# Optimization experiments

Measured on AMD Instinct MI355X. Metric: run time of the kernel, lower is better.

The kernel has to match this reference:

```python
import jax, jax.numpy as jnp
import numpy as np

B, L, D_MODEL = 2, 1024, 1024
D_STATE, D_CONV, EXPAND, HEADDIM = 64, 4, 2, 64
D_INNER = EXPAND * D_MODEL              # 2048
NHEADS = D_INNER // HEADDIM             # 32
NGROUPS = 1
CONV_DIM = D_INNER + 2 * NGROUPS * D_STATE            # 2176
D_IN_PROJ = 2 * D_INNER + 2 * NGROUPS * D_STATE + NHEADS  # 4256
RMS_EPS = 1e-6      # block nn.RMSNorm eps
GATED_EPS = 1e-5    # Mamba2 RMSNormGated eps

def _rmsnorm(x, w, eps):
    return x * jax.lax.rsqrt(jnp.mean(x * x, axis=-1, keepdims=True) + eps) * w

def _silu(x):
    return x * jax.nn.sigmoid(x)

def _mamba2(x, W_in, conv_w, conv_b, dt_bias, A_log, D_param, ssm_norm_w, W_out):
    b, l, _ = x.shape
    zxbcdt = x @ W_in.T                                   # (b,l,D_IN_PROJ)
    z = zxbcdt[..., :D_INNER]
    xBC = zxbcdt[..., D_INNER:D_INNER + CONV_DIM]
    dt = zxbcdt[..., D_INNER + CONV_DIM:]                 # (b,l,H)
    # depthwise causal conv1d (kernel D_CONV) + silu
    pad = jnp.pad(xBC, ((0, 0), (D_CONV - 1, 0), (0, 0)))
    conv = conv_b + sum(pad[:, i:i + l, :] * conv_w[:, i] for i in range(D_CONV))
    xBC = _silu(conv)
    xs = xBC[..., :D_INNER].reshape(b, l, NHEADS, HEADDIM)
    Bm = xBC[..., D_INNER:D_INNER + D_STATE]              # (b,l,N), ngroups=1
    Cm = xBC[..., D_INNER + D_STATE:]                     # (b,l,N)
    dt = jax.nn.softplus(dt + dt_bias)                    # (b,l,H)
    dA = jnp.exp(dt * (-jnp.exp(A_log)))                  # (b,l,H)
    dtx = dt[..., None] * xs                              # (b,l,H,P)

    def step(h, inp):
        dA_t, dtx_t, B_t, C_t = inp
        h = h * dA_t[:, :, None, None] + dtx_t[..., None] * B_t[:, None, None, :]
        y_t = jnp.einsum('bhpn,bn->bhp', h, C_t)
        return h, y_t

    h0 = jnp.zeros((b, NHEADS, HEADDIM, D_STATE), x.dtype)
    _, ys = jax.lax.scan(step, h0, (dA.transpose(1, 0, 2), dtx.transpose(1, 0, 2, 3),
                                    Bm.transpose(1, 0, 2), Cm.transpose(1, 0, 2)))
    y = ys.transpose(1, 0, 2, 3) + xs * D_param[None, None, :, None]
    y = y.reshape(b, l, D_INNER)
    y = _rmsnorm(y * _silu(z), ssm_norm_w, GATED_EPS)     # RMSNormGated, norm_before_gate=False
    return y @ W_out.T

def _block(x, x_d, norm_w, W_in, conv_w, conv_b, dt_bias, A_log, D_param, ssm_norm_w, W_out, w1, w2):
    # dual_residual=True, residual_scale=1.0, dropout is identity (eval)
    x_ln = _rmsnorm(x, norm_w, RMS_EPS)
    x_f = _mamba2(x_ln, W_in, conv_w, conv_b, dt_bias, A_log, D_param, ssm_norm_w, W_out)
    x_a = x + x_f
    x_f_scaled = x_f
    x_ln = _rmsnorm(x_a, norm_w, RMS_EPS)
    g = x_ln @ w1.T
    x_f = (g * jax.nn.sigmoid(g)) * (x_ln @ w2.T)         # SwiGLU
    x_a = x_a + x_f
    x_f_scaled = x_f_scaled + x_f
    return x_a, x_d + x_f_scaled

def setup_inputs() -> dict:
    key = jax.random.key(0)
    ks = jax.random.split(key, 12)
    dt = jax.random.uniform(ks[6], (NHEADS,), minval=1e-3, maxval=0.1)
    return {
        'x': jax.random.normal(ks[0], (B, L, D_MODEL), jnp.float32),
        'x_d': jax.random.normal(ks[1], (B, L, D_MODEL), jnp.float32),
        'norm_w': jnp.ones((D_MODEL,), jnp.float32),
        'W_in': jax.random.normal(ks[2], (D_IN_PROJ, D_MODEL), jnp.float32) * (D_MODEL ** -0.5),
        'conv_w': jax.random.normal(ks[3], (CONV_DIM, D_CONV), jnp.float32) * 0.2,
        'conv_b': jnp.zeros((CONV_DIM,), jnp.float32),
        'dt_bias': dt + jnp.log(-jnp.expm1(-dt)),   # inverse softplus of dt
        'A_log': jnp.log(jax.random.uniform(ks[7], (NHEADS,), minval=1.0, maxval=16.0)),
        'D_param': jnp.ones((NHEADS,), jnp.float32),
        'ssm_norm_w': jnp.ones((D_INNER,), jnp.float32),
        'W_out': jax.random.normal(ks[4], (D_MODEL, D_INNER), jnp.float32) * (D_INNER ** -0.5),
        'w1': jax.random.normal(ks[8], (D_MODEL, D_MODEL), jnp.float32) * (D_MODEL ** -0.5),
        'w2': jax.random.normal(ks[9], (D_MODEL, D_MODEL), jnp.float32) * (D_MODEL ** -0.5),
    }

def reference(x, x_d, norm_w, W_in, conv_w, conv_b, dt_bias, A_log, D_param, ssm_norm_w, W_out, w1, w2):
    return _block(x, x_d, norm_w, W_in, conv_w, conv_b, dt_bias, A_log, D_param, ssm_norm_w, W_out, w1, w2)
```

## Files before the change

kernel.cpp:

```cpp
#include <hip/hip_runtime.h>

typedef unsigned short u16;
typedef __attribute__((ext_vector_type(8))) short bf16x8;
typedef __attribute__((ext_vector_type(4))) float f32x4;

#define B_      2
#define L_      1024
#define DM      1024
#define DI      2048
#define NH      32
#define HD      64
#define DSTATE  64
#define CONVD   2176
#define DPROJ   4256
#define ZXS     4352

__device__ __forceinline__ u16 f2bf(float f) {
  union { float f; unsigned u; } v; v.f = f;
  unsigned r = v.u + 0x7fffu + ((v.u >> 16) & 1u);
  return (u16)(r >> 16);
}
__device__ __forceinline__ float bf2f(u16 b) {
  union { unsigned u; float f; } v; v.u = ((unsigned)b) << 16;
  return v.f;
}

__device__ __forceinline__ void load_lds16(const void* g, void* l) {
  __builtin_amdgcn_global_load_lds(
      (const __attribute__((address_space(1))) void*)g,
      (__attribute__((address_space(3))) void*)l, 16, 0, 0);
}

template<int P> __device__ __forceinline__ void wait_prefetch() {
  if constexpr (P == 4)      asm volatile("s_waitcnt vmcnt(4)\n\ts_barrier" ::: "memory");
  else if constexpr (P == 6) asm volatile("s_waitcnt vmcnt(6)\n\ts_barrier" ::: "memory");
  else if constexpr (P == 8) asm volatile("s_waitcnt vmcnt(8)\n\ts_barrier" ::: "memory");
}

__device__ __forceinline__ float block_reduce_sum256(float v) {
  #pragma unroll
  for (int off = 32; off > 0; off >>= 1) v += __shfl_down(v, off, 64);
  __shared__ float red[4];
  int lane = threadIdx.x & 63, w = threadIdx.x >> 6;
  if (lane == 0) red[w] = v;
  __syncthreads();
  return red[0] + red[1] + red[2] + red[3];
}

__global__ __launch_bounds__(256) void rms_and_convert(
    const float* __restrict__ x, const float* __restrict__ norm_w, u16* __restrict__ xlnb,
    const float* __restrict__ W_in, const float* __restrict__ W_out,
    const float* __restrict__ w1, const float* __restrict__ w2,
    u16* __restrict__ Winb, u16* __restrict__ Woutb, u16* __restrict__ w12b) {
  if (blockIdx.x < 2048) {
    const int row = blockIdx.x;
    const int c = threadIdx.x << 2;
    float4 v = *(const float4*)(x + (long)row * DM + c);
    float ss = v.x * v.x + v.y * v.y + v.z * v.z + v.w * v.w;
    float tot = block_reduce_sum256(ss);
    float sc = rsqrtf(tot * (1.0f / DM) + 1e-6f);
    float4 wv = *(const float4*)(norm_w + c);
    *(ushort4*)(xlnb + (long)row * DM + c) =
        make_ushort4(f2bf(v.x * sc * wv.x), f2bf(v.y * sc * wv.y),
                     f2bf(v.z * sc * wv.z), f2bf(v.w * sc * wv.w));
    return;
  }
  const long R0 = 4256L * 1024 / 4;
  const long R1 = R0 + 2048L * 1024 / 4;
  long i = (long)(blockIdx.x - 2048) * 256 + threadIdx.x;
  float4 v;
  ushort4* dst;
  if (i < R0) {
    v = ((const float4*)W_in)[i];
    dst = ((ushort4*)Winb) + i;
  } else if (i < R1) {
    long j = i - R0;
    v = ((const float4*)W_out)[j];
    dst = ((ushort4*)Woutb) + j;
  } else {
    long j = i - R1;
    long row = j >> 8;
    const float* s = (row < 1024) ? (w1 + row * 1024) : (w2 + (row - 1024) * 1024);
    v = ((const float4*)s)[j & 255];
    dst = ((ushort4*)w12b) + j;
  }
  *dst = make_ushort4(f2bf(v.x), f2bf(v.y), f2bf(v.z), f2bf(v.w));
}

__global__ __launch_bounds__(256) void add_rms_kernel(
    const float* __restrict__ in1, const float* __restrict__ in2,
    float* __restrict__ sum_out, const float* __restrict__ wt,
    u16* __restrict__ out, float eps) {
  const int row = blockIdx.x;
  const int c = threadIdx.x << 2;
  float4 v = *(const float4*)(in1 + (long)row * DM + c);
  float4 u = *(const float4*)(in2 + (long)row * DM + c);
  v.x += u.x; v.y += u.y; v.z += u.z; v.w += u.w;
  *(float4*)(sum_out + (long)row * DM + c) = v;
  float ss = v.x * v.x + v.y * v.y + v.z * v.z + v.w * v.w;
  float tot = block_reduce_sum256(ss);
  float sc = rsqrtf(tot * (1.0f / DM) + eps);
  float4 wv = *(const float4*)(wt + c);
  *(ushort4*)(out + (long)row * DM + c) =
      make_ushort4(f2bf(v.x * sc * wv.x), f2bf(v.y * sc * wv.y),
                   f2bf(v.z * sc * wv.z), f2bf(v.w * sc * wv.w));
}

template<int NI, int NJ, int OUT>
__global__ __launch_bounds__(256) void gemm_lds(
    const u16* __restrict__ A, const u16* __restrict__ Bw,
    void* __restrict__ Cv, int N, int Nw, int Ksub, int Kstride) {
  constexpr int BM = NI * 32;
  constexpr int BN = NJ * 32;
  __shared__ u16 As[2][BM][64];
  __shared__ u16 Bs[2][BN][64];
  const int tid = threadIdx.x;
  const int lane = tid & 63;
  const int wave = tid >> 6;
  const int ml = lane & 15;
  const int quad = lane >> 4;
  const int wm = (wave & 1) * (NI * 16);
  const int wn = (wave >> 1) * (NJ * 16);
  const long bm = (long)blockIdx.y * BM;
  const long bn = (long)blockIdx.x * BN;
  const long koff = (long)blockIdx.z * Ksub;

  const int lr = lane >> 3;
  const int lc = (lane & 7) ^ lr;

  f32x4 acc[NI][NJ];
  #pragma unroll
  for (int i = 0; i < NI; ++i)
    #pragma unroll
    for (int j = 0; j < NJ; ++j)
      acc[i][j] = (f32x4){0.f, 0.f, 0.f, 0.f};

  auto stage = [&](int kk, int buf) {
    #pragma unroll
    for (int t = 0; t < BM / 32; ++t) {
      const int u = wave * (BM / 32) + t;
      load_lds16(A + (bm + u * 8 + lr) * Kstride + koff + kk + lc * 8, &As[buf][u * 8][0]);
    }
    #pragma unroll
    for (int t = 0; t < BN / 32; ++t) {
      const int u = wave * (BN / 32) + t;
      long brow = bn + u * 8 + lr;
      if (brow >= Nw) brow = Nw - 1;
      load_lds16(Bw + brow * Kstride + koff + kk + lc * 8, &Bs[buf][u * 8][0]);
    }
  };

  stage(0, 0);
  int buf = 0;
  for (int kt = 0; kt < Ksub; kt += 64) {
    if (kt + 64 < Ksub) {
      stage(kt + 64, buf ^ 1);
      wait_prefetch<NI + NJ>();
    } else {
      asm volatile("s_waitcnt vmcnt(0)\n\ts_barrier" ::: "memory");
    }
    #pragma unroll
    for (int ks = 0; ks < 2; ++ks) {
      const int c = ks * 4 + quad;
      const int pc = (c ^ (ml & 7)) << 3;
      bf16x8 af[NI], bfr[NJ];
      #pragma unroll
      for (int i = 0; i < NI; ++i)
        af[i] = *(const bf16x8*)&As[buf][wm + (i << 4) + ml][pc];
      #pragma unroll
      for (int j = 0; j < NJ; ++j)
        bfr[j] = *(const bf16x8*)&Bs[buf][wn + (j << 4) + ml][pc];
      #pragma unroll
      for (int i = 0; i < NI; ++i)
        #pragma unroll
        for (int j = 0; j < NJ; ++j)
          acc[i][j] = __builtin_amdgcn_mfma_f32_16x16x32_bf16(af[i], bfr[j], acc[i][j], 0, 0, 0);
    }
    asm volatile("s_barrier" ::: "memory");
    buf ^= 1;
  }

  const int rquad = quad << 2;
  #pragma unroll
  for (int i = 0; i < NI; ++i) {
    const long gm = bm + wm + (i << 4) + rquad;
    #pragma unroll
    for (int j = 0; j < NJ; ++j) {
      const long gn = bn + wn + (j << 4) + ml;
      #pragma unroll
      for (int r = 0; r < 4; ++r) {
        if constexpr (OUT == 0)
          ((float*)Cv)[(gm + r) * N + gn] = acc[i][j][r];
        else if constexpr (OUT == 1)
          ((u16*)Cv)[(gm + r) * N + gn] = f2bf(acc[i][j][r]);
        else
          atomicAdd(&((float*)Cv)[(gm + r) * N + gn], acc[i][j][r]);
      }
    }
  }
}

__global__ __launch_bounds__(256) void gemm_mlp_final(
    const u16* __restrict__ A, const u16* __restrict__ Bw,
    const float* __restrict__ xa, const float* __restrict__ xd,
    const float* __restrict__ xf, float* __restrict__ out, int K) {
  __shared__ u16 As[2][64][64];
  __shared__ u16 Bs[2][128][64];
  const int tid = threadIdx.x;
  const int lane = tid & 63;
  const int wave = tid >> 6;
  const int ml = lane & 15;
  const int quad = lane >> 4;
  const int wm = (wave & 1) * 32;
  const int wn = (wave >> 1) * 32;
  const long bm = (long)blockIdx.y * 64;
  const long c0 = (long)blockIdx.x * 64;

  const int lr = lane >> 3;
  const int lc = (lane & 7) ^ lr;

  f32x4 acc[2][4];
  #pragma unroll
  for (int i = 0; i < 2; ++i)
    #pragma unroll
    for (int j = 0; j < 4; ++j)
      acc[i][j] = (f32x4){0.f, 0.f, 0.f, 0.f};

  auto stage = [&](int kk, int buf) {
    #pragma unroll
    for (int t = 0; t < 2; ++t) {
      const int u = wave * 2 + t;
      load_lds16(A + (bm + u * 8 + lr) * K + kk + lc * 8, &As[buf][u * 8][0]);
    }
    #pragma unroll
    for (int t = 0; t < 4; ++t) {
      const int u = wave * 4 + t;
      const int r = u * 8 + lr;
      const long grow = (r < 64) ? (c0 + r) : (1024 + c0 + (r - 64));
      load_lds16(Bw + grow * K + kk + lc * 8, &Bs[buf][u * 8][0]);
    }
  };

  stage(0, 0);
  int buf = 0;
  for (int kt = 0; kt < K; kt += 64) {
    if (kt + 64 < K) {
      stage(kt + 64, buf ^ 1);
      wait_prefetch<6>();
    } else {
      asm volatile("s_waitcnt vmcnt(0)\n\ts_barrier" ::: "memory");
    }
    #pragma unroll
    for (int ks = 0; ks < 2; ++ks) {
      const int c = ks * 4 + quad;
      const int pc = (c ^ (ml & 7)) << 3;
      bf16x8 af[2], bfr[4];
      #pragma unroll
      for (int i = 0; i < 2; ++i)
        af[i] = *(const bf16x8*)&As[buf][wm + (i << 4) + ml][pc];
      #pragma unroll
      for (int j = 0; j < 2; ++j) {
        bfr[j]     = *(const bf16x8*)&Bs[buf][wn + (j << 4) + ml][pc];
        bfr[j + 2] = *(const bf16x8*)&Bs[buf][64 + wn + (j << 4) + ml][pc];
      }
      #pragma unroll
      for (int i = 0; i < 2; ++i)
        #pragma unroll
        for (int j = 0; j < 4; ++j)
          acc[i][j] = __builtin_amdgcn_mfma_f32_16x16x32_bf16(af[i], bfr[j], acc[i][j], 0, 0, 0);
    }
    asm volatile("s_barrier" ::: "memory");
    buf ^= 1;
  }

  float* out1 = out + (long)B_ * L_ * DM;
  const int rquad = quad << 2;
  #pragma unroll
  for (int i = 0; i < 2; ++i) {
    const long gm = bm + wm + (i << 4) + rquad;
    #pragma unroll
    for (int jj = 0; jj < 2; ++jj) {
      const long col = c0 + wn + (jj << 4) + ml;
      #pragma unroll
      for (int r = 0; r < 4; ++r) {
        float g = acc[i][jj][r];
        float h = acc[i][jj + 2][r];
        float e = (g / (1.f + expf(-g))) * h;
        long o = (gm + r) * DM + col;
        out[o]  = xa[o] + e;
        out1[o] = xd[o] + xf[o] + e;
      }
    }
  }
}

__global__ __launch_bounds__(256) void conv_silu_kernel(
    const u16* __restrict__ zx, const float* __restrict__ cw,
    const float* __restrict__ cb, u16* __restrict__ xc) {
  int idx = blockIdx.x * 256 + threadIdx.x;
  if (idx >= 2048 * 544) return;
  const int c4 = (idx % 544) << 2;
  const int row = idx / 544;
  const int t = row & (L_ - 1);
  float4 acc = *(const float4*)(cb + c4);
  float4 w0 = *(const float4*)(cw + (c4 + 0) * 4);
  float4 w1v = *(const float4*)(cw + (c4 + 1) * 4);
  float4 w2v = *(const float4*)(cw + (c4 + 2) * 4);
  float4 w3v = *(const float4*)(cw + (c4 + 3) * 4);
  const float wts[4][4] = {{w0.x, w0.y, w0.z, w0.w},
                           {w1v.x, w1v.y, w1v.z, w1v.w},
                           {w2v.x, w2v.y, w2v.z, w2v.w},
                           {w3v.x, w3v.y, w3v.z, w3v.w}};
  #pragma unroll
  for (int i = 0; i < 4; ++i) {
    int tau = t - 3 + i;
    if (tau >= 0) {
      ushort4 xb = *(const ushort4*)(zx + (long)(row - t + tau) * ZXS + DI + c4);
      acc.x = fmaf(bf2f(xb.x), wts[0][i], acc.x);
      acc.y = fmaf(bf2f(xb.y), wts[1][i], acc.y);
      acc.z = fmaf(bf2f(xb.z), wts[2][i], acc.z);
      acc.w = fmaf(bf2f(xb.w), wts[3][i], acc.w);
    }
  }
  acc.x = acc.x / (1.f + expf(-acc.x));
  acc.y = acc.y / (1.f + expf(-acc.y));
  acc.z = acc.z / (1.f + expf(-acc.z));
  acc.w = acc.w / (1.f + expf(-acc.w));
  *(ushort4*)(xc + (long)row * CONVD + c4) =
      make_ushort4(f2bf(acc.x), f2bf(acc.y), f2bf(acc.z), f2bf(acc.w));
}

__global__ __launch_bounds__(256) void ssd_chunk_kernel(
    const u16* __restrict__ xc, const u16* __restrict__ zx,
    const float* __restrict__ dt_bias, const float* __restrict__ A_log,
    u16* __restrict__ yss, float* __restrict__ Sbuf,
    float* __restrict__ EGbuf, float* __restrict__ Lam) {
  const int c = blockIdx.x & 15;
  const int h = (blockIdx.x >> 4) & 31;
  const int b = blockIdx.x >> 9;
  const int bh = b * NH + h;
  const long crow = (long)b * L_ + c * 64;
  const int tid = threadIdx.x, lane = tid & 63, wave = tid >> 6;

  __shared__ u16 Cs[64][72], Bs[64][72], Xt[64][72], Btw[64][72], Ms[64][72];
  __shared__ float Gs[64], wjL[64], dtL[64];

  if (wave == 0) {
    float draw = bf2f(zx[(crow + lane) * ZXS + (DI + CONVD) + h]) + dt_bias[h];
    float dt = (draw > 20.f) ? draw : log1pf(expf(draw));
    float g = -expf(A_log[h]) * dt;
    float G = g;
    #pragma unroll
    for (int off = 1; off < 64; off <<= 1) {
      float t = __shfl_up(G, off, 64);
      if (lane >= off) G += t;
    }
    float G63 = __shfl(G, 63, 64);
    Gs[lane] = G;
    wjL[lane] = expf(G63 - G) * dt;
    dtL[lane] = dt;
    EGbuf[(bh * 16 + c) * 64 + lane] = expf(G);
    if (lane == 63) Lam[bh * 16 + c] = expf(G63);
  }
  __syncthreads();
  for (int idx = tid; idx < 1024; idx += 256) {
    int r = idx >> 4, c4 = (idx & 15) << 2;
    const u16* row = xc + (crow + r) * CONVD;
    ushort4 xv = *(const ushort4*)(row + h * HD + c4);
    Xt[c4 + 0][r] = xv.x; Xt[c4 + 1][r] = xv.y;
    Xt[c4 + 2][r] = xv.z; Xt[c4 + 3][r] = xv.w;
    ushort4 bv = *(const ushort4*)(row + DI + c4);
    *(ushort4*)&Bs[r][c4] = bv;
    float w = wjL[r];
    Btw[c4 + 0][r] = f2bf(bf2f(bv.x) * w); Btw[c4 + 1][r] = f2bf(bf2f(bv.y) * w);
    Btw[c4 + 2][r] = f2bf(bf2f(bv.z) * w); Btw[c4 + 3][r] = f2bf(bf2f(bv.w) * w);
    *(ushort4*)&Cs[r][c4] = *(const ushort4*)(row + DI + DSTATE + c4);
  }
  __syncthreads();

  const int mrow = wave * 16 + (lane & 15);
  const int quad = lane >> 4;
  f32x4 accE[4];
  #pragma unroll
  for (int j = 0; j < 4; ++j) accE[j] = (f32x4){0.f, 0.f, 0.f, 0.f};
  #pragma unroll
  for (int ks = 0; ks < 2; ++ks) {
    int k0 = ks * 32 + quad * 8;
    bf16x8 a = *(const bf16x8*)&Cs[mrow][k0];
    #pragma unroll
    for (int j = 0; j < 4; ++j) {
      bf16x8 bfr = *(const bf16x8*)&Bs[j * 16 + (lane & 15)][k0];
      accE[j] = __builtin_amdgcn_mfma_f32_16x16x32_bf16(a, bfr, accE[j], 0, 0, 0);
    }
  }
  #pragma unroll
  for (int j = 0; j < 4; ++j) {
    int jc = j * 16 + (lane & 15);
    float Gj = Gs[jc], dtj = dtL[jc];
    #pragma unroll
    for (int r = 0; r < 4; ++r) {
      int ir = wave * 16 + quad * 4 + r;
      float v = (ir >= jc) ? accE[j][r] * expf(Gs[ir] - Gj) * dtj : 0.f;
      Ms[ir][jc] = f2bf(v);
    }
  }
  __syncthreads();
  f32x4 accY[4], accS[4];
  #pragma unroll
  for (int j = 0; j < 4; ++j) { accY[j] = (f32x4){0.f,0.f,0.f,0.f}; accS[j] = (f32x4){0.f,0.f,0.f,0.f}; }
  #pragma unroll
  for (int ks = 0; ks < 2; ++ks) {
    int k0 = ks * 32 + quad * 8;
    bf16x8 aM = *(const bf16x8*)&Ms[mrow][k0];
    bf16x8 aX = *(const bf16x8*)&Xt[mrow][k0];
    #pragma unroll
    for (int j = 0; j < 4; ++j) {
      bf16x8 bX = *(const bf16x8*)&Xt[j * 16 + (lane & 15)][k0];
      bf16x8 bB = *(const bf16x8*)&Btw[j * 16 + (lane & 15)][k0];
      accY[j] = __builtin_amdgcn_mfma_f32_16x16x32_bf16(aM, bX, accY[j], 0, 0, 0);
      accS[j] = __builtin_amdgcn_mfma_f32_16x16x32_bf16(aX, bB, accS[j], 0, 0, 0);
    }
  }
  float* Sc = Sbuf + (long)(bh * 16 + c) * 4096;
  #pragma unroll
  for (int j = 0; j < 4; ++j) {
    int col = j * 16 + (lane & 15);
    #pragma unroll
    for (int r = 0; r < 4; ++r) {
      int mr = wave * 16 + quad * 4 + r;
      yss[(crow + mr) * DI + h * HD + col] = f2bf(accY[j][r]);
      Sc[mr * 64 + col] = accS[j][r];
    }
  }
}

__global__ __launch_bounds__(256) void ssd_combine_kernel(
    float* __restrict__ Sbuf, const float* __restrict__ Lam) {
  const int bh = blockIdx.x >> 4;
  const int e = (blockIdx.x & 15) * 256 + threadIdx.x;
  float* base = Sbuf + (long)bh * 16 * 4096 + e;
  const float* lamp = Lam + bh * 16;
  float H = 0.f;
  for (int cc = 0; cc < 16; ++cc) {
    float lam = lamp[cc];
    float v = base[cc * 4096];
    base[cc * 4096] = H;
    H = fmaf(lam, H, v);
  }
}

__global__ __launch_bounds__(256) void ssd_final_kernel(
    const u16* __restrict__ xc, const float* __restrict__ Sbuf,
    const float* __restrict__ EGbuf, const float* __restrict__ Dp,
    u16* __restrict__ yss) {
  const int c = blockIdx.x & 15;
  const int h = (blockIdx.x >> 4) & 31;
  const int b = blockIdx.x >> 9;
  const int bh = b * NH + h;
  const long crow = (long)b * L_ + c * 64;
  const int tid = threadIdx.x, lane = tid & 63, wave = tid >> 6;
  __shared__ u16 Csc[64][72], Hs[64][72];
  __shared__ float egL[64];
  if (tid < 64) egL[tid] = EGbuf[(bh * 16 + c) * 64 + tid];
  __syncthreads();
  const float* Sc = Sbuf + (long)(bh * 16 + c) * 4096;
  for (int idx = tid; idx < 1024; idx += 256) {
    int r = idx >> 4, c4 = (idx & 15) << 2;
    float4 hv = *(const float4*)(Sc + r * 64 + c4);
    *(ushort4*)&Hs[r][c4] = make_ushort4(f2bf(hv.x), f2bf(hv.y), f2bf(hv.z), f2bf(hv.w));
    float eg = egL[r];
    ushort4 cv = *(const ushort4*)(xc + (crow + r) * CONVD + DI + DSTATE + c4);
    *(ushort4*)&Csc[r][c4] = make_ushort4(f2bf(bf2f(cv.x) * eg), f2bf(bf2f(cv.y) * eg),
                                          f2bf(bf2f(cv.z) * eg), f2bf(bf2f(cv.w) * eg));
  }
  __syncthreads();
  const int mrow = wave * 16 + (lane & 15);
  const int quad = lane >> 4;
  f32x4 acc[4];
  #pragma unroll
  for (int j = 0; j < 4; ++j) acc[j] = (f32x4){0.f, 0.f, 0.f, 0.f};
  #pragma unroll
  for (int ks = 0; ks < 2; ++ks) {
    int k0 = ks * 32 + quad * 8;
    bf16x8 a = *(const bf16x8*)&Csc[mrow][k0];
    #pragma unroll
    for (int j = 0; j < 4; ++j) {
      bf16x8 bfr = *(const bf16x8*)&Hs[j * 16 + (lane & 15)][k0];
      acc[j] = __builtin_amdgcn_mfma_f32_16x16x32_bf16(a, bfr, acc[j], 0, 0, 0);
    }
  }
  const float Dh = Dp[h];
  #pragma unroll
  for (int j = 0; j < 4; ++j) {
    int p = j * 16 + (lane & 15);
    #pragma unroll
    for (int r = 0; r < 4; ++r) {
      int ir = wave * 16 + quad * 4 + r;
      long o = (crow + ir) * DI + h * HD + p;
      float xval = bf2f(xc[(crow + ir) * CONVD + h * HD + p]);
      yss[o] = f2bf(bf2f(yss[o]) + acc[j][r] + Dh * xval);
    }
  }
}

__global__ __launch_bounds__(256) void gated_rms_kernel(
    const u16* __restrict__ y, const u16* __restrict__ zx,
    const float* __restrict__ wt, u16* __restrict__ out,
    float* __restrict__ xf_zero) {
  const int row = blockIdx.x;
  const int c = threadIdx.x << 3;
  const u16* yr = y + (long)row * DI + c;
  const u16* zr = zx + (long)row * ZXS + c;
  *(float4*)(xf_zero + (long)row * DM + (threadIdx.x << 2)) = make_float4(0.f, 0.f, 0.f, 0.f);
  float v[8];
  float ss = 0.f;
  #pragma unroll
  for (int i = 0; i < 8; i += 4) {
    ushort4 y4 = *(const ushort4*)(yr + i);
    ushort4 z4 = *(const ushort4*)(zr + i);
    const float zz[4] = {bf2f(z4.x), bf2f(z4.y), bf2f(z4.z), bf2f(z4.w)};
    const float yy[4] = {bf2f(y4.x), bf2f(y4.y), bf2f(y4.z), bf2f(y4.w)};
    #pragma unroll
    for (int j = 0; j < 4; ++j) {
      float sg = zz[j] / (1.f + expf(-zz[j]));
      float val = yy[j] * sg;
      v[i + j] = val;
      ss += val * val;
    }
  }
  float tot = block_reduce_sum256(ss);
  float sc = rsqrtf(tot * (1.0f / DI) + 1e-5f);
  const float* wr = wt + c;
  *(ushort4*)(out + (long)row * DI + c) =
      make_ushort4(f2bf(v[0] * sc * wr[0]), f2bf(v[1] * sc * wr[1]),
                   f2bf(v[2] * sc * wr[2]), f2bf(v[3] * sc * wr[3]));
  *(ushort4*)(out + (long)row * DI + c + 4) =
      make_ushort4(f2bf(v[4] * sc * wr[4]), f2bf(v[5] * sc * wr[5]),
                   f2bf(v[6] * sc * wr[6]), f2bf(v[7] * sc * wr[7]));
}

extern "C" void kernel_launch(void* const* d_in, const int* in_sizes, int n_in,
                              void* d_out, int out_size, void* d_ws, size_t ws_size,
                              hipStream_t stream) {
  const float* x        = (const float*)d_in[0];
  const float* x_d      = (const float*)d_in[1];
  const float* norm_w   = (const float*)d_in[2];
  const float* W_in     = (const float*)d_in[3];
  const float* conv_w   = (const float*)d_in[4];
  const float* conv_b   = (const float*)d_in[5];
  const float* dt_bias  = (const float*)d_in[6];
  const float* A_log    = (const float*)d_in[7];
  const float* D_param  = (const float*)d_in[8];
  const float* ssm_w    = (const float*)d_in[9];
  const float* W_out    = (const float*)d_in[10];
  const float* w1       = (const float*)d_in[11];
  const float* w2       = (const float*)d_in[12];
  float* out = (float*)d_out;

  char* wsc = (char*)d_ws;
  size_t off = 0;
  auto alloc = [&](size_t n) { char* p = wsc + off; off += (n + 255) & ~(size_t)255; return p; };
  u16*   zx   = (u16*)alloc((size_t)2048 * ZXS * 2);
  u16*   xc   = (u16*)alloc((size_t)2048 * 2176 * 2);
  u16*   yss  = (u16*)alloc((size_t)2048 * 2048 * 2);
  float* xf   = (float*)alloc((size_t)2048 * 1024 * 4);
  float* xa   = (float*)alloc((size_t)2048 * 1024 * 4);
  float* Sbuf = (float*)alloc((size_t)64 * 16 * 4096 * 4);
  float* EGbuf= (float*)alloc((size_t)65536 * 4);
  float* Lam  = (float*)alloc((size_t)1024 * 4);
  u16* xlnb   = (u16*)alloc((size_t)2048 * 1024 * 2);
  u16* ygnb   = (u16*)alloc((size_t)2048 * 2048 * 2);
  u16* xln2b  = (u16*)alloc((size_t)2048 * 1024 * 2);
  u16* Winb   = (u16*)alloc((size_t)4256 * 1024 * 2);
  u16* Woutb  = (u16*)alloc((size_t)1024 * 2048 * 2);
  u16* w12b   = (u16*)alloc((size_t)2048 * 1024 * 2);

  rms_and_convert<<<2048 + 8352, 256, 0, stream>>>(x, norm_w, xlnb,
      W_in, W_out, w1, w2, Winb, Woutb, w12b);
  gemm_lds<4, 2, 1><<<dim3(68, 16), 256, 0, stream>>>(xlnb, Winb, zx, ZXS, 4256, 1024, 1024);
  conv_silu_kernel<<<(2048 * 544 + 255) / 256, 256, 0, stream>>>(zx, conv_w, conv_b, xc);
  ssd_chunk_kernel<<<1024, 256, 0, stream>>>(xc, zx, dt_bias, A_log, yss, Sbuf, EGbuf, Lam);
  ssd_combine_kernel<<<1024, 256, 0, stream>>>(Sbuf, Lam);
  ssd_final_kernel<<<1024, 256, 0, stream>>>(xc, Sbuf, EGbuf, D_param, yss);
  gated_rms_kernel<<<2048, 256, 0, stream>>>(yss, zx, ssm_w, ygnb, xf);
  gemm_lds<2, 2, 2><<<dim3(16, 32, 2), 256, 0, stream>>>(ygnb, Woutb, xf, 1024, 1024, 1024, 2048);
  add_rms_kernel<<<2048, 256, 0, stream>>>(x, xf, xa, norm_w, xln2b, 1e-6f);
  gemm_mlp_final<<<dim3(16, 32), 256, 0, stream>>>(xln2b, w12b, xa, x_d, xf, out, 1024);
}
```

Measured before the change: 255.0 us.

## Fuse conv, chunked SSD, state carry and output into one decoupled-lookback kernel

Replaces the separate conv+silu, chunk, combine and final SSD kernels with a single kernel. It computes the causal conv inline into shared memory, takes chunk order from an atomic ticket, and passes inter-chunk states through a global carry buffer guarded by acquire/release flags. It also drops the xa residual buffer by recomputing x + xf in the final MLP epilogue. This removes several launches and the round trips through xc, Sbuf and EGbuf, at the cost of a serial chain of flag waits across the 16 chunks per head and redundant conv halo loads.

```diff
diff --git a/kernel.cpp b/kernel.cpp
--- a/kernel.cpp
+++ b/kernel.cpp
@@ -89,14 +89,12 @@
 
 __global__ __launch_bounds__(256) void add_rms_kernel(
     const float* __restrict__ in1, const float* __restrict__ in2,
-    float* __restrict__ sum_out, const float* __restrict__ wt,
-    u16* __restrict__ out, float eps) {
+    const float* __restrict__ wt, u16* __restrict__ out, float eps) {
   const int row = blockIdx.x;
   const int c = threadIdx.x << 2;
   float4 v = *(const float4*)(in1 + (long)row * DM + c);
   float4 u = *(const float4*)(in2 + (long)row * DM + c);
   v.x += u.x; v.y += u.y; v.z += u.z; v.w += u.w;
-  *(float4*)(sum_out + (long)row * DM + c) = v;
   float ss = v.x * v.x + v.y * v.y + v.z * v.z + v.w * v.w;
   float tot = block_reduce_sum256(ss);
   float sc = rsqrtf(tot * (1.0f / DM) + eps);
@@ -202,7 +200,7 @@
 
 __global__ __launch_bounds__(256) void gemm_mlp_final(
     const u16* __restrict__ A, const u16* __restrict__ Bw,
-    const float* __restrict__ xa, const float* __restrict__ xd,
+    const float* __restrict__ x0, const float* __restrict__ xd,
     const float* __restrict__ xf, float* __restrict__ out, int K) {
   __shared__ u16 As[2][64][64];
   __shared__ u16 Bs[2][128][64];
@@ -287,63 +285,34 @@
         float h = acc[i][jj + 2][r];
         float e = (g / (1.f + expf(-g))) * h;
         long o = (gm + r) * DM + col;
-        out[o]  = xa[o] + e;
-        out1[o] = xd[o] + xf[o] + e;
-      }
-    }
-  }
-}
-
-__global__ __launch_bounds__(256) void conv_silu_kernel(
-    const u16* __restrict__ zx, const float* __restrict__ cw,
-    const float* __restrict__ cb, u16* __restrict__ xc) {
-  int idx = blockIdx.x * 256 + threadIdx.x;
-  if (idx >= 2048 * 544) return;
-  const int c4 = (idx % 544) << 2;
-  const int row = idx / 544;
-  const int t = row & (L_ - 1);
-  float4 acc = *(const float4*)(cb + c4);
-  float4 w0 = *(const float4*)(cw + (c4 + 0) * 4);
-  float4 w1v = *(const float4*)(cw + (c4 + 1) * 4);
-  float4 w2v = *(const float4*)(cw + (c4 + 2) * 4);
-  float4 w3v = *(const float4*)(cw + (c4 + 3) * 4);
-  const float wts[4][4] = {{w0.x, w0.y, w0.z, w0.w},
-                           {w1v.x, w1v.y, w1v.z, w1v.w},
-                           {w2v.x, w2v.y, w2v.z, w2v.w},
-                           {w3v.x, w3v.y, w3v.z, w3v.w}};
-  #pragma unroll
-  for (int i = 0; i < 4; ++i) {
-    int tau = t - 3 + i;
-    if (tau >= 0) {
-      ushort4 xb = *(const ushort4*)(zx + (long)(row - t + tau) * ZXS + DI + c4);
-      acc.x = fmaf(bf2f(xb.x), wts[0][i], acc.x);
-      acc.y = fmaf(bf2f(xb.y), wts[1][i], acc.y);
-      acc.z = fmaf(bf2f(xb.z), wts[2][i], acc.z);
-      acc.w = fmaf(bf2f(xb.w), wts[3][i], acc.w);
-    }
-  }
-  acc.x = acc.x / (1.f + expf(-acc.x));
-  acc.y = acc.y / (1.f + expf(-acc.y));
-  acc.z = acc.z / (1.f + expf(-acc.z));
-  acc.w = acc.w / (1.f + expf(-acc.w));
-  *(ushort4*)(xc + (long)row * CONVD + c4) =
-      make_ushort4(f2bf(acc.x), f2bf(acc.y), f2bf(acc.z), f2bf(acc.w));
-}
-
-__global__ __launch_bounds__(256) void ssd_chunk_kernel(
-    const u16* __restrict__ xc, const u16* __restrict__ zx,
-    const float* __restrict__ dt_bias, const float* __restrict__ A_log,
-    u16* __restrict__ yss, float* __restrict__ Sbuf,
-    float* __restrict__ EGbuf, float* __restrict__ Lam) {
-  const int c = blockIdx.x & 15;
-  const int h = (blockIdx.x >> 4) & 31;
-  const int b = blockIdx.x >> 9;
+        float f = xf[o];
+        out[o]  = x0[o] + f + e;
+        out1[o] = xd[o] + f + e;
+      }
+    }
+  }
+}
+
+__global__ __launch_bounds__(256) void ssd_fused_kernel(
+    const u16* __restrict__ zx, const float* __restrict__ dt_bias,
+    const float* __restrict__ A_log, const float* __restrict__ cw,
+    const float* __restrict__ cb, const float* __restrict__ Dp,
+    u16* __restrict__ yss, float* __restrict__ carry,
+    int* __restrict__ flags, int* __restrict__ ticket) {
+  __shared__ u16 Cs[64][72], Bs[64][72], Xt[64][72], Btw[64][72], Ms[64][72];
+  __shared__ float Gs[64], wjL[64], dtL[64], egL[64];
+  __shared__ int tickL;
+  const int tid = threadIdx.x, lane = tid & 63, wave = tid >> 6;
+
+  if (tid == 0) tickL = atomicAdd(ticket, 1);
+  __syncthreads();
+  const int tick = tickL;
+  const int c = tick & 15;
+  const int h = (tick >> 4) & 31;
+  const int b = tick >> 9;
   const int bh = b * NH + h;
-  const long crow = (long)b * L_ + c * 64;
-  const int tid = threadIdx.x, lane = tid & 63, wave = tid >> 6;
-
-  __shared__ u16 Cs[64][72], Bs[64][72], Xt[64][72], Btw[64][72], Ms[64][72];
-  __shared__ float Gs[64], wjL[64], dtL[64];
+  const long zrow0 = (long)b * L_;
+  const long crow = zrow0 + c * 64;
 
   if (wave == 0) {
     float draw = bf2f(zx[(crow + lane) * ZXS + (DI + CONVD) + h]) + dt_bias[h];
@@ -357,28 +326,64 @@
     }
     float G63 = __shfl(G, 63, 64);
     Gs[lane] = G;
+    egL[lane] = expf(G);
     wjL[lane] = expf(G63 - G) * dt;
     dtL[lane] = dt;
-    EGbuf[(bh * 16 + c) * 64 + lane] = expf(G);
-    if (lane == 63) Lam[bh * 16 + c] = expf(G63);
   }
   __syncthreads();
-  for (int idx = tid; idx < 1024; idx += 256) {
-    int r = idx >> 4, c4 = (idx & 15) << 2;
-    const u16* row = xc + (crow + r) * CONVD;
-    ushort4 xv = *(const ushort4*)(row + h * HD + c4);
-    Xt[c4 + 0][r] = xv.x; Xt[c4 + 1][r] = xv.y;
-    Xt[c4 + 2][r] = xv.z; Xt[c4 + 3][r] = xv.w;
-    ushort4 bv = *(const ushort4*)(row + DI + c4);
-    *(ushort4*)&Bs[r][c4] = bv;
-    float w = wjL[r];
-    Btw[c4 + 0][r] = f2bf(bf2f(bv.x) * w); Btw[c4 + 1][r] = f2bf(bf2f(bv.y) * w);
-    Btw[c4 + 2][r] = f2bf(bf2f(bv.z) * w); Btw[c4 + 3][r] = f2bf(bf2f(bv.w) * w);
-    *(ushort4*)&Cs[r][c4] = *(const ushort4*)(row + DI + DSTATE + c4);
+
+  for (int idx = tid; idx < 3072; idx += 256) {
+    int r = idx / 48;
+    int g = idx % 48;
+    int t = c * 64 + r;
+    long zcol;
+    if (g < 16)      zcol = DI + (long)h * HD + (g << 2);
+    else if (g < 32) zcol = DI + DI + ((g - 16) << 2);
+    else             zcol = DI + DI + DSTATE + ((g - 32) << 2);
+    int cc = (int)(zcol - DI);
+    float4 acc = *(const float4*)(cb + cc);
+    float4 wv0 = *(const float4*)(cw + (cc + 0) * 4);
+    float4 wv1 = *(const float4*)(cw + (cc + 1) * 4);
+    float4 wv2 = *(const float4*)(cw + (cc + 2) * 4);
+    float4 wv3 = *(const float4*)(cw + (cc + 3) * 4);
+    const float wt0[4] = {wv0.x, wv0.y, wv0.z, wv0.w};
+    const float wt1[4] = {wv1.x, wv1.y, wv1.z, wv1.w};
+    const float wt2[4] = {wv2.x, wv2.y, wv2.z, wv2.w};
+    const float wt3[4] = {wv3.x, wv3.y, wv3.z, wv3.w};
+    #pragma unroll
+    for (int i = 0; i < 4; ++i) {
+      int tau = t - 3 + i;
+      if (tau >= 0) {
+        ushort4 xb = *(const ushort4*)(zx + (zrow0 + tau) * ZXS + zcol);
+        acc.x = fmaf(bf2f(xb.x), wt0[i], acc.x);
+        acc.y = fmaf(bf2f(xb.y), wt1[i], acc.y);
+        acc.z = fmaf(bf2f(xb.z), wt2[i], acc.z);
+        acc.w = fmaf(bf2f(xb.w), wt3[i], acc.w);
+      }
+    }
+    acc.x = acc.x / (1.f + expf(-acc.x));
+    acc.y = acc.y / (1.f + expf(-acc.y));
+    acc.z = acc.z / (1.f + expf(-acc.z));
+    acc.w = acc.w / (1.f + expf(-acc.w));
+    if (g < 16) {
+      int k = g << 2;
+      Xt[k + 0][r] = f2bf(acc.x); Xt[k + 1][r] = f2bf(acc.y);
+      Xt[k + 2][r] = f2bf(acc.z); Xt[k + 3][r] = f2bf(acc.w);
+    } else if (g < 32) {
+      int n = (g - 16) << 2;
+      *(ushort4*)&Bs[r][n] = make_ushort4(f2bf(acc.x), f2bf(acc.y), f2bf(acc.z), f2bf(acc.w));
+      float w = wjL[r];
+      Btw[n + 0][r] = f2bf(acc.x * w); Btw[n + 1][r] = f2bf(acc.y * w);
+      Btw[n + 2][r] = f2bf(acc.z * w); Btw[n + 3][r] = f2bf(acc.w * w);
+    } else {
+      int n = (g - 32) << 2;
+      *(ushort4*)&Cs[r][n] = make_ushort4(f2bf(acc.x), f2bf(acc.y), f2bf(acc.z), f2bf(acc.w));
+    }
   }
   __syncthreads();
 
-  const int mrow = wave * 16 + (lane & 15);
+  const int ml = lane & 15;
+  const int mrow = wave * 16 + ml;
   const int quad = lane >> 4;
   f32x4 accE[4];
   #pragma unroll
@@ -389,13 +394,13 @@
     bf16x8 a = *(const bf16x8*)&Cs[mrow][k0];
     #pragma unroll
     for (int j = 0; j < 4; ++j) {
-      bf16x8 bfr = *(const bf16x8*)&Bs[j * 16 + (lane & 15)][k0];
+      bf16x8 bfr = *(const bf16x8*)&Bs[j * 16 + ml][k0];
       accE[j] = __builtin_amdgcn_mfma_f32_16x16x32_bf16(a, bfr, accE[j], 0, 0, 0);
     }
   }
   #pragma unroll
   for (int j = 0; j < 4; ++j) {
-    int jc = j * 16 + (lane & 15);
+    int jc = j * 16 + ml;
     float Gj = Gs[jc], dtj = dtL[jc];
     #pragma unroll
     for (int r = 0; r < 4; ++r) {
@@ -415,90 +420,90 @@
     bf16x8 aX = *(const bf16x8*)&Xt[mrow][k0];
     #pragma unroll
     for (int j = 0; j < 4; ++j) {
-      bf16x8 bX = *(const bf16x8*)&Xt[j * 16 + (lane & 15)][k0];
-      bf16x8 bB = *(const bf16x8*)&Btw[j * 16 + (lane & 15)][k0];
+      bf16x8 bX = *(const bf16x8*)&Xt[j * 16 + ml][k0];
+      bf16x8 bB = *(const bf16x8*)&Btw[j * 16 + ml][k0];
       accY[j] = __builtin_amdgcn_mfma_f32_16x16x32_bf16(aM, bX, accY[j], 0, 0, 0);
       accS[j] = __builtin_amdgcn_mfma_f32_16x16x32_bf16(aX, bB, accS[j], 0, 0, 0);
     }
   }
-  float* Sc = Sbuf + (long)(bh * 16 + c) * 4096;
+
+  const float lam = egL[63];
+  float* myslot = carry + (long)(bh * 16 + c) * 4096;
+  float Hin[4][4];
+  if (c > 0) {
+    float* prev = carry + (long)(bh * 16 + c - 1) * 4096;
+    int* fl = flags + bh * 16 + (c - 1);
+    if (tid == 0) {
+      while (__hip_atomic_load(fl, __ATOMIC_ACQUIRE, __HIP_MEMORY_SCOPE_AGENT) == 0)
+        __builtin_amdgcn_s_sleep(2);
+    }
+    __syncthreads();
+    #pragma unroll
+    for (int j = 0; j < 4; ++j) {
+      int n = j * 16 + ml;
+      #pragma unroll
+      for (int r = 0; r < 4; ++r) {
+        int p = wave * 16 + quad * 4 + r;
+        Hin[j][r] = __hip_atomic_load(prev + p * 64 + n, __ATOMIC_RELAXED, __HIP_MEMORY_SCOPE_AGENT);
+      }
+    }
+  } else {
+    #pragma unroll
+    for (int j = 0; j < 4; ++j)
+      #pragma unroll
+      for (int r = 0; r < 4; ++r) Hin[j][r] = 0.f;
+  }
   #pragma unroll
   for (int j = 0; j < 4; ++j) {
-    int col = j * 16 + (lane & 15);
+    int n = j * 16 + ml;
     #pragma unroll
     for (int r = 0; r < 4; ++r) {
-      int mr = wave * 16 + quad * 4 + r;
-      yss[(crow + mr) * DI + h * HD + col] = f2bf(accY[j][r]);
-      Sc[mr * 64 + col] = accS[j][r];
-    }
-  }
-}
-
-__global__ __launch_bounds__(256) void ssd_combine_kernel(
-    float* __restrict__ Sbuf, const float* __restrict__ Lam) {
-  const int bh = blockIdx.x >> 4;
-  const int e = (blockIdx.x & 15) * 256 + threadIdx.x;
-  float* base = Sbuf + (long)bh * 16 * 4096 + e;
-  const float* lamp = Lam + bh * 16;
-  float H = 0.f;
-  for (int cc = 0; cc < 16; ++cc) {
-    float lam = lamp[cc];
-    float v = base[cc * 4096];
-    base[cc * 4096] = H;
-    H = fmaf(lam, H, v);
-  }
-}
-
-__global__ __launch_bounds__(256) void ssd_final_kernel(
-    const u16* __restrict__ xc, const float* __restrict__ Sbuf,
-    const float* __restrict__ EGbuf, const float* __restrict__ Dp,
-    u16* __restrict__ yss) {
-  const int c = blockIdx.x & 15;
-  const int h = (blockIdx.x >> 4) & 31;
-  const int b = blockIdx.x >> 9;
-  const int bh = b * NH + h;
-  const long crow = (long)b * L_ + c * 64;
-  const int tid = threadIdx.x, lane = tid & 63, wave = tid >> 6;
-  __shared__ u16 Csc[64][72], Hs[64][72];
-  __shared__ float egL[64];
-  if (tid < 64) egL[tid] = EGbuf[(bh * 16 + c) * 64 + tid];
+      int p = wave * 16 + quad * 4 + r;
+      float hout = fmaf(lam, Hin[j][r], accS[j][r]);
+      __hip_atomic_store(myslot + p * 64 + n, hout, __ATOMIC_RELAXED, __HIP_MEMORY_SCOPE_AGENT);
+    }
+  }
+  __threadfence();
   __syncthreads();
-  const float* Sc = Sbuf + (long)(bh * 16 + c) * 4096;
-  for (int idx = tid; idx < 1024; idx += 256) {
-    int r = idx >> 4, c4 = (idx & 15) << 2;
-    float4 hv = *(const float4*)(Sc + r * 64 + c4);
-    *(ushort4*)&Hs[r][c4] = make_ushort4(f2bf(hv.x), f2bf(hv.y), f2bf(hv.z), f2bf(hv.w));
-    float eg = egL[r];
-    ushort4 cv = *(const ushort4*)(xc + (crow + r) * CONVD + DI + DSTATE + c4);
-    *(ushort4*)&Csc[r][c4] = make_ushort4(f2bf(bf2f(cv.x) * eg), f2bf(bf2f(cv.y) * eg),
-                                          f2bf(bf2f(cv.z) * eg), f2bf(bf2f(cv.w) * eg));
-  }
-  __syncthreads();
-  const int mrow = wave * 16 + (lane & 15);
-  const int quad = lane >> 4;
-  f32x4 acc[4];
-  #pragma unroll
-  for (int j = 0; j < 4; ++j) acc[j] = (f32x4){0.f, 0.f, 0.f, 0.f};
-  #pragma unroll
-  for (int ks = 0; ks < 2; ++ks) {
-    int k0 = ks * 32 + quad * 8;
-    bf16x8 a = *(const bf16x8*)&Csc[mrow][k0];
+  if (tid == 0)
+    __hip_atomic_store(flags + bh * 16 + c, 1, __ATOMIC_RELEASE, __HIP_MEMORY_SCOPE_AGENT);
+
+  f32x4 accI[4];
+  #pragma unroll
+  for (int j = 0; j < 4; ++j) accI[j] = (f32x4){0.f, 0.f, 0.f, 0.f};
+  if (c > 0) {
     #pragma unroll
     for (int j = 0; j < 4; ++j) {
-      bf16x8 bfr = *(const bf16x8*)&Hs[j * 16 + (lane & 15)][k0];
-      acc[j] = __builtin_amdgcn_mfma_f32_16x16x32_bf16(a, bfr, acc[j], 0, 0, 0);
-    }
-  }
+      int n = j * 16 + ml;
+      #pragma unroll
+      for (int r = 0; r < 4; ++r) {
+        int p = wave * 16 + quad * 4 + r;
+        Ms[p][n] = f2bf(Hin[j][r]);
+      }
+    }
+    __syncthreads();
+    #pragma unroll
+    for (int ks = 0; ks < 2; ++ks) {
+      int k0 = ks * 32 + quad * 8;
+      bf16x8 a = *(const bf16x8*)&Cs[mrow][k0];
+      #pragma unroll
+      for (int j = 0; j < 4; ++j) {
+        bf16x8 bfr = *(const bf16x8*)&Ms[j * 16 + ml][k0];
+        accI[j] = __builtin_amdgcn_mfma_f32_16x16x32_bf16(a, bfr, accI[j], 0, 0, 0);
+      }
+    }
+  }
+
   const float Dh = Dp[h];
   #pragma unroll
   for (int j = 0; j < 4; ++j) {
-    int p = j * 16 + (lane & 15);
+    int p = j * 16 + ml;
     #pragma unroll
     for (int r = 0; r < 4; ++r) {
-      int ir = wave * 16 + quad * 4 + r;
-      long o = (crow + ir) * DI + h * HD + p;
-      float xval = bf2f(xc[(crow + ir) * CONVD + h * HD + p]);
-      yss[o] = f2bf(bf2f(yss[o]) + acc[j][r] + Dh * xval);
+      int i = wave * 16 + quad * 4 + r;
+      float xval = bf2f(Xt[p][i]);
+      float y = accY[j][r] + egL[i] * accI[j][r] + Dh * xval;
+      yss[(crow + i) * DI + (long)h * HD + p] = f2bf(y);
     }
   }
 }
@@ -561,29 +566,26 @@
   size_t off = 0;
   auto alloc = [&](size_t n) { char* p = wsc + off; off += (n + 255) & ~(size_t)255; return p; };
   u16*   zx   = (u16*)alloc((size_t)2048 * ZXS * 2);
-  u16*   xc   = (u16*)alloc((size_t)2048 * 2176 * 2);
   u16*   yss  = (u16*)alloc((size_t)2048 * 2048 * 2);
   float* xf   = (float*)alloc((size_t)2048 * 1024 * 4);
-  float* xa   = (float*)alloc((size_t)2048 * 1024 * 4);
-  float* Sbuf = (float*)alloc((size_t)64 * 16 * 4096 * 4);
-  float* EGbuf= (float*)alloc((size_t)65536 * 4);
-  float* Lam  = (float*)alloc((size_t)1024 * 4);
+  float* carry= (float*)alloc((size_t)64 * 16 * 4096 * 4);
+  int*   flags= (int*)alloc((size_t)1028 * 4);
   u16* xlnb   = (u16*)alloc((size_t)2048 * 1024 * 2);
   u16* ygnb   = (u16*)alloc((size_t)2048 * 2048 * 2);
   u16* xln2b  = (u16*)alloc((size_t)2048 * 1024 * 2);
   u16* Winb   = (u16*)alloc((size_t)4256 * 1024 * 2);
   u16* Woutb  = (u16*)alloc((size_t)1024 * 2048 * 2);
   u16* w12b   = (u16*)alloc((size_t)2048 * 1024 * 2);
-
+  int* ticket = flags + 1024;
+
+  hipMemsetAsync(flags, 0, 1028 * 4, stream);
   rms_and_convert<<<2048 + 8352, 256, 0, stream>>>(x, norm_w, xlnb,
       W_in, W_out, w1, w2, Winb, Woutb, w12b);
   gemm_lds<4, 2, 1><<<dim3(68, 16), 256, 0, stream>>>(xlnb, Winb, zx, ZXS, 4256, 1024, 1024);
-  conv_silu_kernel<<<(2048 * 544 + 255) / 256, 256, 0, stream>>>(zx, conv_w, conv_b, xc);
-  ssd_chunk_kernel<<<1024, 256, 0, stream>>>(xc, zx, dt_bias, A_log, yss, Sbuf, EGbuf, Lam);
-  ssd_combine_kernel<<<1024, 256, 0, stream>>>(Sbuf, Lam);
-  ssd_final_kernel<<<1024, 256, 0, stream>>>(xc, Sbuf, EGbuf, D_param, yss);
+  ssd_fused_kernel<<<1024, 256, 0, stream>>>(zx, dt_bias, A_log, conv_w, conv_b,
+                                             D_param, yss, carry, flags, ticket);
   gated_rms_kernel<<<2048, 256, 0, stream>>>(yss, zx, ssm_w, ygnb, xf);
   gemm_lds<2, 2, 2><<<dim3(16, 32, 2), 256, 0, stream>>>(ygnb, Woutb, xf, 1024, 1024, 1024, 2048);
-  add_rms_kernel<<<2048, 256, 0, stream>>>(x, xf, xa, norm_w, xln2b, 1e-6f);
-  gemm_mlp_final<<<dim3(16, 32), 256, 0, stream>>>(xln2b, w12b, xa, x_d, xf, out, 1024);
-}
+  add_rms_kernel<<<2048, 256, 0, stream>>>(x, xf, norm_w, xln2b, 1e-6f);
+  gemm_mlp_final<<<dim3(16, 32), 256, 0, stream>>>(xln2b, w12b, x, x_d, xf, out, 1024);
+}
```

New measurement: 824.7 us. +223.4%, slower.
